# Kernel optimization log

Measured on AMD Instinct MI355X. Metric: run time of the kernel, lower is better.

Reference implementation:

```python
import jax, jax.numpy as jnp
import numpy as np

NHEAD = 16
HEAD_DIM = 64
ROPE_BASE = 10000.0


def _rotate_half(x):
    # interleaved convention: pairs (x0,x1)->(-x1,x0)
    x1 = x[..., ::2]
    x2 = x[..., 1::2]
    return jnp.stack([-x2, x1], axis=-1).reshape(x.shape)


def _rope_cache(seq_len, head_dim, base):
    half = head_dim // 2
    inv_freq = 1.0 / base ** (jnp.arange(half, dtype=jnp.float32) / float(half))
    t = jnp.arange(seq_len, dtype=jnp.float32)
    freqs = jnp.einsum('i,j->ij', t, inv_freq)          # [T, half]
    emb = jnp.concatenate([freqs, freqs], axis=-1)      # [T, D] (half-half cat, matches torch source)
    return jnp.cos(emb), jnp.sin(emb)


def setup_inputs() -> dict:
    key = jax.random.key(0)
    k1, k2, k3 = jax.random.split(key, 3)
    b, t, c = 2, 2048, 1024
    x = jax.random.normal(k1, (b, t, c), dtype=jnp.float32)
    # torch nn.Linear weights: [out_features, in_features], scaled like kaiming-uniform-ish
    W_qkv = jax.random.normal(k2, (3 * c, c), dtype=jnp.float32) / np.sqrt(c)
    W_out = jax.random.normal(k3, (c, c), dtype=jnp.float32) / np.sqrt(c)
    return {"x": x, "W_qkv": W_qkv, "W_out": W_out}


def reference(x, W_qkv, W_out):
    b, t, c = x.shape
    nh, hd = NHEAD, HEAD_DIM
    qkv = x @ W_qkv.T                                   # [b, t, 3c]
    q, k, v = jnp.split(qkv, 3, axis=-1)

    def to_heads(a):
        return a.reshape(b, t, nh, hd).transpose(0, 2, 1, 3)  # [b, nh, t, hd]

    q, k, v = to_heads(q), to_heads(k), to_heads(v)
    cos, sin = _rope_cache(t, hd, ROPE_BASE)            # [t, hd]
    cos = cos.astype(q.dtype)[None, None]
    sin = sin.astype(q.dtype)[None, None]
    q = q * cos + _rotate_half(q) * sin
    k = k * cos + _rotate_half(k) * sin

    scale = 1.0 / np.sqrt(hd).astype(np.float32)
    scores = jnp.einsum('bhqd,bhkd->bhqk', q, k) * scale
    attn = jax.nn.softmax(scores, axis=-1)
    y = jnp.einsum('bhqk,bhkd->bhqd', attn, v)          # [b, nh, t, hd]
    y = y.transpose(0, 2, 1, 3).reshape(b, t, c)
    return y @ W_out.T
```

## Files before the change

### kernel.cpp

```cpp
#include <hip/hip_runtime.h>
#include <hip/hip_bf16.h>
#include <math.h>

typedef __hip_bfloat16 bf16;
typedef _Float16 f16;
typedef __attribute__((ext_vector_type(8))) short bf16x8;
typedef __attribute__((ext_vector_type(8))) _Float16 f16x8;
typedef __attribute__((ext_vector_type(4))) float f32x4;
typedef __attribute__((ext_vector_type(4))) unsigned u32x4;

#define MFMA_BF(a,b,c) __builtin_amdgcn_mfma_f32_16x16x32_bf16((a),(b),(c),0,0,0)
#define MFMA_F16(a,b,c) __builtin_amdgcn_mfma_f32_16x16x32_f16((a),(b),(c),0,0,0)

__device__ __forceinline__ void load_lds16(const void* g, void* l) {
  __builtin_amdgcn_global_load_lds(
      (__attribute__((address_space(1))) void*)(g),
      (__attribute__((address_space(3))) void*)(l), 16, 0, 0);
}

__device__ __forceinline__ unsigned pk_bf16(float a, float b) {
  unsigned ua = __builtin_bit_cast(unsigned, a);
  unsigned ub = __builtin_bit_cast(unsigned, b);
  ua += 0x7fffu + ((ua >> 16) & 1u);
  ub += 0x7fffu + ((ub >> 16) & 1u);
  return (ua >> 16) | (ub & 0xffff0000u);
}

__global__ void cvt_all(const float* __restrict__ x, const float* __restrict__ wq,
                        const float* __restrict__ wo, unsigned* __restrict__ xb,
                        unsigned* __restrict__ wqb, unsigned* __restrict__ wob) {
  int i = blockIdx.x * blockDim.x + threadIdx.x;
  const float* src;
  unsigned* dst;
  int off;
  if (i < 1048576) { src = x; dst = xb; off = i; }
  else if (i < 1048576 + 786432) { src = wq; dst = wqb; off = i - 1048576; }
  else { src = wo; dst = wob; off = i - (1048576 + 786432); }
  float4 v = reinterpret_cast<const float4*>(src)[off];
  uint2 u;
  u.x = pk_bf16(v.x, v.y);
  u.y = pk_bf16(v.z, v.w);
  reinterpret_cast<uint2*>(dst)[off] = u;
}

__global__ __launch_bounds__(256, 3)
void gemm_qkv(const bf16* __restrict__ A, const bf16* __restrict__ B,
              bf16* __restrict__ outq, bf16* __restrict__ outk,
              f16* __restrict__ outv) {
  __shared__ __align__(16) bf16 As[3][128 * 32];
  __shared__ __align__(16) bf16 Bs[3][128 * 32];
  const int K = 1024;
  const int tid = threadIdx.x;
  const int w = tid >> 6;
  const int lane = tid & 63;
  const int quad = lane >> 4;
  const int col = lane & 15;
  const int waveM = w >> 1;
  const int waveN = w & 1;
  const int bm = blockIdx.y * 128;
  const int bn = blockIdx.x * 128;

  f32x4 acc[4][4] = {};
  const int srow = lane >> 2;
  const int skoff = (((lane & 3) ^ ((srow >> 1) & 3))) * 8;
  const int swq = (quad ^ ((col >> 1) & 3)) * 8;

  auto stage = [&](int k0, int sb) {
#pragma unroll
    for (int p = 0; p < 2; ++p) {
      int r = p * 64 + w * 16 + srow;
      load_lds16(A + (size_t)(bm + r) * K + k0 + skoff,
                 (char*)As + sb * 8192 + p * 4096 + w * 1024);
      load_lds16(B + (size_t)(bn + r) * K + k0 + skoff,
                 (char*)Bs + sb * 8192 + p * 4096 + w * 1024);
    }
  };

  stage(0, 0);
  stage(32, 1);

  int cb = 0;
  for (int k0 = 0; k0 < K; k0 += 32) {
    if (k0 + 32 < K) __asm__ volatile("s_waitcnt vmcnt(4)" ::: "memory");
    else             __asm__ volatile("s_waitcnt vmcnt(0)" ::: "memory");
    __asm__ volatile("s_barrier" ::: "memory");
    if (k0 + 64 < K) {
      int nb = cb + 2; if (nb >= 3) nb -= 3;
      stage(k0 + 64, nb);
    }
    const bf16* at = &As[cb][0];
    const bf16* bt = &Bs[cb][0];
    bf16x8 af[4], bfr[4];
#pragma unroll
    for (int i = 0; i < 4; ++i)
      af[i] = *reinterpret_cast<const bf16x8*>(at + (waveM * 64 + i * 16 + col) * 32 + swq);
#pragma unroll
    for (int j = 0; j < 4; ++j)
      bfr[j] = *reinterpret_cast<const bf16x8*>(bt + (waveN * 64 + j * 16 + col) * 32 + swq);
#pragma unroll
    for (int i = 0; i < 4; ++i)
#pragma unroll
      for (int j = 0; j < 4; ++j)
        acc[i][j] = MFMA_BF(af[i], bfr[j], acc[i][j]);
    cb = (cb == 2) ? 0 : cb + 1;
  }

  if (bn < 2048) {
    const float NEGK = -0.4152410118f;
    const float C1 = 0.1803368799f;
    const float sgn = (col & 1) ? 1.0f : -1.0f;
#pragma unroll
    for (int j = 0; j < 4; ++j) {
      const int n0 = bn + waveN * 64 + j * 16;
      const int sel = n0 >> 10;
      const int hh = (n0 & 1023) >> 6;
      const int dd = (n0 & 63) + col;
      bf16* outp = sel ? outk : outq;
      const float post = sel ? 1.0f : C1;
      const float invf = __builtin_amdgcn_exp2f((float)((n0 & 31) + col) * NEGK);
#pragma unroll
      for (int i = 0; i < 4; ++i) {
#pragma unroll
        for (int r = 0; r < 4; ++r) {
          int m = bm + waveM * 64 + i * 16 + quad * 4 + r;
          int b = m >> 11, t = m & 2047;
          float v = acc[i][j][r];
          float partner = __shfl_xor(v, 1);
          float ang = (float)t * invf;
          float res = (v * __cosf(ang) + sgn * partner * __sinf(ang)) * post;
          outp[((size_t)(b * 16 + hh) * 2048 + t) * 64 + dd] = __float2bfloat16(res);
        }
      }
    }
  } else {
    const int b = bm >> 11;
    const int tt0 = (bm & 2047) + waveM * 64;
#pragma unroll
    for (int j = 0; j < 4; ++j) {
      const int n0 = bn + waveN * 64 + j * 16;
      const int hh = (n0 & 1023) >> 6;
      const int dd = (n0 & 63) + col;
      f16* dst = outv + (size_t)(b * 16 + hh) * 131072 + (size_t)dd * 2048;
#pragma unroll
      for (int i = 0; i < 4; ++i) {
        uint2 pk;
        pk.x = __builtin_bit_cast(unsigned, __builtin_amdgcn_cvt_pkrtz(acc[i][j][0], acc[i][j][1]));
        pk.y = __builtin_bit_cast(unsigned, __builtin_amdgcn_cvt_pkrtz(acc[i][j][2], acc[i][j][3]));
        *reinterpret_cast<uint2*>(dst + tt0 + i * 16 + quad * 4) = pk;
      }
    }
  }
}

__global__ __launch_bounds__(512, 2)
void gemm_out(const bf16* __restrict__ A, const bf16* __restrict__ B,
              float* __restrict__ outf) {
  __shared__ __align__(16) bf16 As[3][128 * 32];
  __shared__ __align__(16) bf16 Bs[3][128 * 32];
  const int K = 1024;
  const int tid = threadIdx.x;
  const int w = tid >> 6;
  const int lane = tid & 63;
  const int quad = lane >> 4;
  const int col = lane & 15;
  const int waveM = w >> 2;
  const int waveN = w & 3;
  const int bm = blockIdx.y * 128;
  const int bn = blockIdx.x * 128;

  f32x4 acc[4][2] = {};
  const int srow = lane >> 2;
  const int skoff = (((lane & 3) ^ ((srow >> 1) & 3))) * 8;
  const int swq = (quad ^ ((col >> 1) & 3)) * 8;

  auto stage = [&](int k0, int sb) {
    int r = w * 16 + srow;
    load_lds16(A + (size_t)(bm + r) * K + k0 + skoff,
               (char*)As + sb * 8192 + w * 1024);
    load_lds16(B + (size_t)(bn + r) * K + k0 + skoff,
               (char*)Bs + sb * 8192 + w * 1024);
  };

  stage(0, 0);
  stage(32, 1);

  int cb = 0;
  for (int k0 = 0; k0 < K; k0 += 32) {
    if (k0 + 32 < K) __asm__ volatile("s_waitcnt vmcnt(2)" ::: "memory");
    else             __asm__ volatile("s_waitcnt vmcnt(0)" ::: "memory");
    __asm__ volatile("s_barrier" ::: "memory");
    if (k0 + 64 < K) {
      int nb = cb + 2; if (nb >= 3) nb -= 3;
      stage(k0 + 64, nb);
    }
    const bf16* at = &As[cb][0];
    const bf16* bt = &Bs[cb][0];
    bf16x8 af[4], bfr[2];
#pragma unroll
    for (int i = 0; i < 4; ++i)
      af[i] = *reinterpret_cast<const bf16x8*>(at + (waveM * 64 + i * 16 + col) * 32 + swq);
#pragma unroll
    for (int j = 0; j < 2; ++j)
      bfr[j] = *reinterpret_cast<const bf16x8*>(bt + (waveN * 32 + j * 16 + col) * 32 + swq);
#pragma unroll
    for (int i = 0; i < 4; ++i)
#pragma unroll
      for (int j = 0; j < 2; ++j)
        acc[i][j] = MFMA_BF(af[i], bfr[j], acc[i][j]);
    cb = (cb == 2) ? 0 : cb + 1;
  }

#pragma unroll
  for (int i = 0; i < 4; ++i)
#pragma unroll
    for (int j = 0; j < 2; ++j) {
      const int n0 = bn + waveN * 32 + j * 16;
#pragma unroll
      for (int r = 0; r < 4; ++r) {
        int m = bm + waveM * 64 + i * 16 + quad * 4 + r;
        outf[(size_t)m * 1024 + n0 + col] = acc[i][j][r];
      }
    }
}

__global__ __launch_bounds__(256, 2)
void attn_kernel(const bf16* __restrict__ qh, const bf16* __restrict__ kh,
                 const f16* __restrict__ vt, bf16* __restrict__ y) {
  __shared__ __align__(16) bf16 Ks[2][2 * 64 * 64];
  __shared__ __align__(16) f16 Vs[3][2 * 64 * 64];

  const int bh = blockIdx.x;
  const int qt = blockIdx.y;
  const int w = threadIdx.x >> 6;
  const int lane = threadIdx.x & 63;
  const int quad = lane >> 4;
  const int col = lane & 15;

  const int qrow0 = qt * 128 + w * 32 + col;
  bf16x8 qf[2][2];
#pragma unroll
  for (int f = 0; f < 2; ++f)
#pragma unroll
    for (int c = 0; c < 2; ++c)
      qf[f][c] = *reinterpret_cast<const bf16x8*>(
          qh + ((size_t)bh * 2048 + qrow0 + f * 16) * 64 + c * 32 + quad * 8);

  const int s8 = lane >> 3;
  const int blk = (lane & 7) ^ s8;
  const bf16* kg = kh + (size_t)bh * 2048 * 64;
  const f16* vg = vt + (size_t)bh * 64 * 2048;
  const int ks0 = 32 * (w >> 1) + 8 * ((4 * w + (s8 >> 2)) & 3) + 4 * (w & 1) + (s8 & 3);
  const int ks1 = 32 * (w >> 1) + 8 * ((4 * w + 2 + (s8 >> 2)) & 3) + 4 * (w & 1) + (s8 & 3);
  const int vrow0 = w * 16 + s8;

  const int csw = col & 7;
  const int sw0 = (quad ^ csw) * 8;
  const int sw1 = ((quad + 4) ^ csw) * 8;
  const int rdbase = col * 64;

  f32x4 O[2][4] = {};
  float l[2] = {};
  f16x8 pf[2][4];

  auto stageK2 = [&](int kn, int kb) {
    char* kbp = (char*)Ks + kb * 16384 + w * 2048;
    load_lds16(kg + (size_t)(kn + ks0) * 64 + blk * 8, kbp);
    load_lds16(kg + (size_t)(kn + ks1) * 64 + blk * 8, kbp + 1024);
    load_lds16(kg + (size_t)(kn + 64 + ks0) * 64 + blk * 8, kbp + 8192);
    load_lds16(kg + (size_t)(kn + 64 + ks1) * 64 + blk * 8, kbp + 8192 + 1024);
  };
  auto stageV2 = [&](int kn, int vb) {
    char* vbp = (char*)Vs + vb * 16384 + w * 2048;
    load_lds16(vg + (size_t)vrow0 * 2048 + kn + blk * 8, vbp);
    load_lds16(vg + (size_t)(vrow0 + 8) * 2048 + kn + blk * 8, vbp + 1024);
    load_lds16(vg + (size_t)vrow0 * 2048 + kn + 64 + blk * 8, vbp + 8192);
    load_lds16(vg + (size_t)(vrow0 + 8) * 2048 + kn + 64 + blk * 8, vbp + 8192 + 1024);
  };

  auto softmax = [&](f32x4 (&s)[2][2][4]) {
#pragma unroll
    for (int f = 0; f < 2; ++f) {
      unsigned pk[16];
      float lf = 0.0f;
#pragma unroll
      for (int u = 0; u < 2; ++u)
#pragma unroll
        for (int t = 0; t < 4; ++t) {
          float p0 = __builtin_amdgcn_exp2f(s[f][u][t][0]);
          float p1 = __builtin_amdgcn_exp2f(s[f][u][t][1]);
          float p2 = __builtin_amdgcn_exp2f(s[f][u][t][2]);
          float p3 = __builtin_amdgcn_exp2f(s[f][u][t][3]);
          lf += (p0 + p1) + (p2 + p3);
          pk[u * 8 + t * 2]     = __builtin_bit_cast(unsigned, __builtin_amdgcn_cvt_pkrtz(p0, p1));
          pk[u * 8 + t * 2 + 1] = __builtin_bit_cast(unsigned, __builtin_amdgcn_cvt_pkrtz(p2, p3));
        }
      l[f] += lf;
      pf[f][0] = __builtin_bit_cast(f16x8, (u32x4){pk[0], pk[1], pk[2], pk[3]});
      pf[f][1] = __builtin_bit_cast(f16x8, (u32x4){pk[4], pk[5], pk[6], pk[7]});
      pf[f][2] = __builtin_bit_cast(f16x8, (u32x4){pk[8], pk[9], pk[10], pk[11]});
      pf[f][3] = __builtin_bit_cast(f16x8, (u32x4){pk[12], pk[13], pk[14], pk[15]});
    }
  };

  stageK2(0, 0);
  stageV2(0, 0);

  __asm__ volatile("s_waitcnt vmcnt(4)" ::: "memory");
  __asm__ volatile("s_barrier" ::: "memory");
  stageK2(128, 1);
  stageV2(128, 1);
  {
    f32x4 s[2][2][4];
    __builtin_amdgcn_s_setprio(1);
#pragma unroll
    for (int u = 0; u < 2; ++u) {
      const bf16* kt = &Ks[0][u * 4096];
#pragma unroll
      for (int t = 0; t < 4; ++t) {
        bf16x8 kf0 = *reinterpret_cast<const bf16x8*>(kt + t * 1024 + rdbase + sw0);
        bf16x8 kf1 = *reinterpret_cast<const bf16x8*>(kt + t * 1024 + rdbase + sw1);
#pragma unroll
        for (int f = 0; f < 2; ++f) {
          f32x4 a = {};
          a = MFMA_BF(kf0, qf[f][0], a);
          a = MFMA_BF(kf1, qf[f][1], a);
          s[f][u][t] = a;
        }
      }
    }
    __builtin_amdgcn_s_setprio(0);
    softmax(s);
  }

  int vprev = 0;
  int vnext = 2;
#pragma unroll 1
  for (int c = 1; c < 16; ++c) {
    const int kc = c * 128;
    __asm__ volatile("s_waitcnt vmcnt(4)" ::: "memory");
    __asm__ volatile("s_barrier" ::: "memory");
    if (c + 1 < 16) {
      stageK2(kc + 128, (c + 1) & 1);
      stageV2(kc + 128, vnext);
    }

    f32x4 s[2][2][4];
    __builtin_amdgcn_s_setprio(1);
#pragma unroll
    for (int u = 0; u < 2; ++u) {
      const bf16* kt = &Ks[c & 1][u * 4096];
      const f16* vtile = &Vs[vprev][u * 4096];
#pragma unroll
      for (int t = 0; t < 4; ++t) {
        bf16x8 kf0 = *reinterpret_cast<const bf16x8*>(kt + t * 1024 + rdbase + sw0);
        bf16x8 kf1 = *reinterpret_cast<const bf16x8*>(kt + t * 1024 + rdbase + sw1);
        f16x8 vf0 = *reinterpret_cast<const f16x8*>(vtile + t * 1024 + rdbase + sw0);
        f16x8 vf1 = *reinterpret_cast<const f16x8*>(vtile + t * 1024 + rdbase + sw1);
#pragma unroll
        for (int f = 0; f < 2; ++f) {
          f32x4 a = {};
          a = MFMA_BF(kf0, qf[f][0], a);
          a = MFMA_BF(kf1, qf[f][1], a);
          s[f][u][t] = a;
          O[f][t] = MFMA_F16(vf0, pf[f][u * 2], O[f][t]);
          O[f][t] = MFMA_F16(vf1, pf[f][u * 2 + 1], O[f][t]);
        }
      }
    }
    __builtin_amdgcn_s_setprio(0);
    softmax(s);

    vprev = (vprev == 2) ? 0 : vprev + 1;
    vnext = (vnext == 2) ? 0 : vnext + 1;
  }

  __asm__ volatile("s_waitcnt vmcnt(0)" ::: "memory");
  __asm__ volatile("s_barrier" ::: "memory");
  {
    __builtin_amdgcn_s_setprio(1);
#pragma unroll
    for (int u = 0; u < 2; ++u) {
      const f16* vtile = &Vs[vprev][u * 4096];
#pragma unroll
      for (int t = 0; t < 4; ++t) {
        f16x8 vf0 = *reinterpret_cast<const f16x8*>(vtile + t * 1024 + rdbase + sw0);
        f16x8 vf1 = *reinterpret_cast<const f16x8*>(vtile + t * 1024 + rdbase + sw1);
#pragma unroll
        for (int f = 0; f < 2; ++f) {
          O[f][t] = MFMA_F16(vf0, pf[f][u * 2], O[f][t]);
          O[f][t] = MFMA_F16(vf1, pf[f][u * 2 + 1], O[f][t]);
        }
      }
    }
    __builtin_amdgcn_s_setprio(0);
  }

  const int b = bh >> 4, h = bh & 15;
#pragma unroll
  for (int f = 0; f < 2; ++f) {
    float lv = l[f];
    lv += __shfl_xor(lv, 16, 64);
    lv += __shfl_xor(lv, 32, 64);
    float inv = 1.0f / lv;
    int tq = qt * 128 + w * 32 + f * 16 + col;
    size_t base = ((size_t)b * 2048 + tq) * 1024 + h * 64;
#pragma unroll
    for (int j = 0; j < 4; ++j) {
      uint2 pk2;
      pk2.x = pk_bf16(O[f][j][0] * inv, O[f][j][1] * inv);
      pk2.y = pk_bf16(O[f][j][2] * inv, O[f][j][3] * inv);
      *reinterpret_cast<uint2*>((unsigned short*)y + base + j * 16 + quad * 4) = pk2;
    }
  }
}

extern "C" void kernel_launch(void* const* d_in, const int* in_sizes, int n_in,
                              void* d_out, int out_size, void* d_ws, size_t ws_size,
                              hipStream_t stream) {
  const float* x    = (const float*)d_in[0];
  const float* wqkv = (const float*)d_in[1];
  const float* wout = (const float*)d_in[2];
  float* out = (float*)d_out;
  char* ws = (char*)d_ws;

  bf16* xb    = (bf16*)(ws);
  bf16* wqkvb = (bf16*)(ws + (size_t)(8 << 20));
  bf16* woutb = (bf16*)(ws + (size_t)(14 << 20));
  bf16* qh    = (bf16*)(ws + (size_t)(16 << 20));
  bf16* kh    = (bf16*)(ws + (size_t)(24 << 20));
  f16*  vt    = (f16*) (ws + (size_t)(32 << 20));
  bf16* y     = (bf16*)(ws);

  cvt_all<<<8192, 256, 0, stream>>>(x, wqkv, wout,
                                    (unsigned*)xb, (unsigned*)wqkvb, (unsigned*)woutb);
  gemm_qkv<<<dim3(24, 32), 256, 0, stream>>>(xb, wqkvb, qh, kh, vt);
  attn_kernel<<<dim3(32, 16), 256, 0, stream>>>(qh, kh, vt, y);
  gemm_out<<<dim3(8, 32), 512, 0, stream>>>(y, woutb, out);
}
```

Measured before the change: 174.5 us.

## Fuse fp32-to-bf16 conversion into QKV GEMM loads and drop the convert kernel

Removes the separate conversion kernel. The QKV GEMM now loads fp32 x and W_qkv straight into registers, packs them to bf16 and writes them into LDS, using register-staged double buffering in place of the triple-buffered async global-to-LDS copies. The W_out conversion is folded into the tail of the QKV GEMM as a grid-stride loop. This saves one launch and the bf16 write and re-read of the inputs. In exchange, the GEMM reads twice as many global bytes on each tile reload (24 column blocks each re-read x in fp32), spends ALU on conversion inside the main loop, and loses the async load path, which may reduce overlap.

```diff
diff --git a/kernel.cpp b/kernel.cpp
--- a/kernel.cpp
+++ b/kernel.cpp
@@ -26,29 +26,13 @@
   return (ua >> 16) | (ub & 0xffff0000u);
 }
 
-__global__ void cvt_all(const float* __restrict__ x, const float* __restrict__ wq,
-                        const float* __restrict__ wo, unsigned* __restrict__ xb,
-                        unsigned* __restrict__ wqb, unsigned* __restrict__ wob) {
-  int i = blockIdx.x * blockDim.x + threadIdx.x;
-  const float* src;
-  unsigned* dst;
-  int off;
-  if (i < 1048576) { src = x; dst = xb; off = i; }
-  else if (i < 1048576 + 786432) { src = wq; dst = wqb; off = i - 1048576; }
-  else { src = wo; dst = wob; off = i - (1048576 + 786432); }
-  float4 v = reinterpret_cast<const float4*>(src)[off];
-  uint2 u;
-  u.x = pk_bf16(v.x, v.y);
-  u.y = pk_bf16(v.z, v.w);
-  reinterpret_cast<uint2*>(dst)[off] = u;
-}
-
 __global__ __launch_bounds__(256, 3)
-void gemm_qkv(const bf16* __restrict__ A, const bf16* __restrict__ B,
+void gemm_qkv(const float* __restrict__ A, const float* __restrict__ B,
+              const float* __restrict__ Wo,
               bf16* __restrict__ outq, bf16* __restrict__ outk,
-              f16* __restrict__ outv) {
-  __shared__ __align__(16) bf16 As[3][128 * 32];
-  __shared__ __align__(16) bf16 Bs[3][128 * 32];
+              f16* __restrict__ outv, bf16* __restrict__ woutb) {
+  __shared__ __align__(16) bf16 As[2][128 * 32];
+  __shared__ __align__(16) bf16 Bs[2][128 * 32];
   const int K = 1024;
   const int tid = threadIdx.x;
   const int w = tid >> 6;
@@ -65,29 +49,46 @@
   const int skoff = (((lane & 3) ^ ((srow >> 1) & 3))) * 8;
   const int swq = (quad ^ ((col >> 1) & 3)) * 8;
 
-  auto stage = [&](int k0, int sb) {
+  float4 rA[2][2], rB[2][2];
+
+  auto issue = [&](int k0) {
 #pragma unroll
     for (int p = 0; p < 2; ++p) {
       int r = p * 64 + w * 16 + srow;
-      load_lds16(A + (size_t)(bm + r) * K + k0 + skoff,
-                 (char*)As + sb * 8192 + p * 4096 + w * 1024);
-      load_lds16(B + (size_t)(bn + r) * K + k0 + skoff,
-                 (char*)Bs + sb * 8192 + p * 4096 + w * 1024);
-    }
-  };
-
-  stage(0, 0);
-  stage(32, 1);
+      const float4* pa = reinterpret_cast<const float4*>(A + (size_t)(bm + r) * K + k0 + skoff);
+      rA[p][0] = pa[0];
+      rA[p][1] = pa[1];
+      const float4* pb = reinterpret_cast<const float4*>(B + (size_t)(bn + r) * K + k0 + skoff);
+      rB[p][0] = pb[0];
+      rB[p][1] = pb[1];
+    }
+  };
+  auto writeLds = [&](int sb) {
+#pragma unroll
+    for (int p = 0; p < 2; ++p) {
+      uint4 ua, ub;
+      ua.x = pk_bf16(rA[p][0].x, rA[p][0].y);
+      ua.y = pk_bf16(rA[p][0].z, rA[p][0].w);
+      ua.z = pk_bf16(rA[p][1].x, rA[p][1].y);
+      ua.w = pk_bf16(rA[p][1].z, rA[p][1].w);
+      *reinterpret_cast<uint4*>((char*)As + sb * 8192 + p * 4096 + w * 1024 + lane * 16) = ua;
+      ub.x = pk_bf16(rB[p][0].x, rB[p][0].y);
+      ub.y = pk_bf16(rB[p][0].z, rB[p][0].w);
+      ub.z = pk_bf16(rB[p][1].x, rB[p][1].y);
+      ub.w = pk_bf16(rB[p][1].z, rB[p][1].w);
+      *reinterpret_cast<uint4*>((char*)Bs + sb * 8192 + p * 4096 + w * 1024 + lane * 16) = ub;
+    }
+  };
+
+  issue(0);
+  writeLds(0);
+  issue(32);
 
   int cb = 0;
   for (int k0 = 0; k0 < K; k0 += 32) {
-    if (k0 + 32 < K) __asm__ volatile("s_waitcnt vmcnt(4)" ::: "memory");
-    else             __asm__ volatile("s_waitcnt vmcnt(0)" ::: "memory");
+    __asm__ volatile("s_waitcnt lgkmcnt(0)" ::: "memory");
     __asm__ volatile("s_barrier" ::: "memory");
-    if (k0 + 64 < K) {
-      int nb = cb + 2; if (nb >= 3) nb -= 3;
-      stage(k0 + 64, nb);
-    }
+
     const bf16* at = &As[cb][0];
     const bf16* bt = &Bs[cb][0];
     bf16x8 af[4], bfr[4];
@@ -102,7 +103,12 @@
 #pragma unroll
       for (int j = 0; j < 4; ++j)
         acc[i][j] = MFMA_BF(af[i], bfr[j], acc[i][j]);
-    cb = (cb == 2) ? 0 : cb + 1;
+
+    if (k0 + 32 < K) {
+      writeLds(cb ^ 1);
+      if (k0 + 64 < K) issue(k0 + 64);
+    }
+    cb ^= 1;
   }
 
   if (bn < 2048) {
@@ -148,6 +154,17 @@
         pk.y = __builtin_bit_cast(unsigned, __builtin_amdgcn_cvt_pkrtz(acc[i][j][2], acc[i][j][3]));
         *reinterpret_cast<uint2*>(dst + tt0 + i * 16 + quad * 4) = pk;
       }
+    }
+  }
+
+  {
+    int gid = (blockIdx.y * gridDim.x + blockIdx.x) * 256 + tid;
+    for (int i = gid; i < 262144; i += 196608) {
+      float4 v = reinterpret_cast<const float4*>(Wo)[i];
+      uint2 u;
+      u.x = pk_bf16(v.x, v.y);
+      u.y = pk_bf16(v.z, v.w);
+      reinterpret_cast<uint2*>(woutb)[i] = u;
     }
   }
 }
@@ -423,17 +440,13 @@
   float* out = (float*)d_out;
   char* ws = (char*)d_ws;
 
-  bf16* xb    = (bf16*)(ws);
-  bf16* wqkvb = (bf16*)(ws + (size_t)(8 << 20));
-  bf16* woutb = (bf16*)(ws + (size_t)(14 << 20));
-  bf16* qh    = (bf16*)(ws + (size_t)(16 << 20));
-  bf16* kh    = (bf16*)(ws + (size_t)(24 << 20));
-  f16*  vt    = (f16*) (ws + (size_t)(32 << 20));
-  bf16* y     = (bf16*)(ws);
-
-  cvt_all<<<8192, 256, 0, stream>>>(x, wqkv, wout,
-                                    (unsigned*)xb, (unsigned*)wqkvb, (unsigned*)woutb);
-  gemm_qkv<<<dim3(24, 32), 256, 0, stream>>>(xb, wqkvb, qh, kh, vt);
+  bf16* woutb = (bf16*)(ws);
+  bf16* qh    = (bf16*)(ws + (size_t)(2 << 20));
+  bf16* kh    = (bf16*)(ws + (size_t)(10 << 20));
+  f16*  vt    = (f16*) (ws + (size_t)(18 << 20));
+  bf16* y     = (bf16*)(ws + (size_t)(26 << 20));
+
+  gemm_qkv<<<dim3(24, 32), 256, 0, stream>>>(x, wqkv, wout, qh, kh, vt, woutb);
   attn_kernel<<<dim3(32, 16), 256, 0, stream>>>(qh, kh, vt, y);
   gemm_out<<<dim3(8, 32), 512, 0, stream>>>(y, woutb, out);
 }
```

After: 183.2 us. 5.0% more time.
